# Optimization experiments

Hardware: AMD Instinct MI355X
Metric: run time of the kernel (lower is better)

The kernel has to match this reference:

```python
import jax, jax.numpy as jnp
import numpy as np

N = 100000   # nodes
E = 1600000  # edges
D_IN, H1, H2, H3 = 128, 128, 128, 64


def _sage_layer(x, src, dst, Wl, Wr, b):
    # PyG SAGEConv (aggr='mean'): out = lin_l(mean_{j in N(i)} x_j) + lin_r(x_i)
    msg_sum = jax.ops.segment_sum(x[src], dst, num_segments=N)          # [N, F]
    deg = jax.ops.segment_sum(jnp.ones((src.shape[0],), x.dtype), dst, num_segments=N)
    mean = msg_sum / jnp.clip(deg, 1.0)[:, None]
    return mean @ Wl + x @ Wr + b


def setup_inputs() -> dict:
    key = jax.random.key(0)
    ks = jax.random.split(key, 11)
    x = jax.random.normal(ks[0], (N, D_IN), dtype=jnp.float32)
    edge_index = jax.random.randint(ks[1], (2, E), 0, N, dtype=jnp.int32)

    def w(k, fin, fout):
        return jax.random.normal(k, (fin, fout), dtype=jnp.float32) * (1.0 / np.sqrt(fin))

    return {
        "x": x,
        "edge_index": edge_index,
        "W1_l": w(ks[2], D_IN, H1), "W1_r": w(ks[3], D_IN, H1), "b1": jnp.zeros((H1,), jnp.float32),
        "W2_l": w(ks[4], H1, H2),  "W2_r": w(ks[5], H1, H2),  "b2": jnp.zeros((H2,), jnp.float32),
        "W3_l": w(ks[6], H2, H3),  "W3_r": w(ks[7], H2, H3),  "b3": jnp.zeros((H3,), jnp.float32),
    }


def reference(x, edge_index, W1_l, W1_r, b1, W2_l, W2_r, b2, W3_l, W3_r, b3):
    src, dst = edge_index[0], edge_index[1]
    h = jax.nn.relu(_sage_layer(x, src, dst, W1_l, W1_r, b1))
    h = jax.nn.relu(_sage_layer(h, src, dst, W2_l, W2_r, b2))
    return _sage_layer(h, src, dst, W3_l, W3_r, b3)
```

## Files before the change

kernel.cpp:

```cpp
#include <hip/hip_runtime.h>

#define NN 100000
#define NE 1600000
#define NPB 256
#define NB 391
#define CAP 4864
#define NBLK_A 512
#define CHUNK_A (NE / NBLK_A)
#define CVT_N (NN * 16)

typedef __attribute__((ext_vector_type(8))) short bf16x8;
typedef __attribute__((ext_vector_type(4))) float f32x4;


__device__ __forceinline__ unsigned short f2bf(float f) {
    unsigned int u = __float_as_uint(f);
    unsigned int r = u + 0x7fffu + ((u >> 16) & 1u);
    return (unsigned short)(r >> 16);
}
__device__ __forceinline__ float bflo(unsigned int u) { return __uint_as_float(u << 16); }
__device__ __forceinline__ float bfhi(unsigned int u) { return __uint_as_float(u & 0xffff0000u); }
__device__ __forceinline__ unsigned int packbf(float lo, float hi) {
    return ((unsigned int)f2bf(hi) << 16) | (unsigned int)f2bf(lo);
}
__device__ __forceinline__ bf16x8 as_bf8(uint4 u) {
    union { uint4 u; bf16x8 h; } c;
    c.u = u;
    return c.h;
}


__global__ __launch_bounds__(256) void bucket_scatter_kernel(
    const int* __restrict__ src, const int* __restrict__ dst,
    int* __restrict__ gcur, unsigned* __restrict__ buckets) {
    __shared__ int hist[NB];
    __shared__ int base[NB];
    int t = threadIdx.x;
    for (int b = t; b < NB; b += 256) hist[b] = 0;
    __syncthreads();
    int e0 = blockIdx.x * CHUNK_A;
    for (int e = e0 + t; e < e0 + CHUNK_A; e += 256)
        atomicAdd(&hist[dst[e] >> 8], 1);
    __syncthreads();
    for (int b = t; b < NB; b += 256) {
        base[b] = atomicAdd(&gcur[b], hist[b]);
        hist[b] = 0;
    }
    __syncthreads();
    for (int e = e0 + t; e < e0 + CHUNK_A; e += 256) {
        int d = dst[e];
        int bkt = d >> 8;
        int slot = base[bkt] + atomicAdd(&hist[bkt], 1);
        if (slot < CAP)
            buckets[(size_t)bkt * CAP + slot] =
                ((unsigned)(d & 255) << 24) | (unsigned)src[e];
    }
}


__global__ __launch_bounds__(512) void bucket_scan_kernel(
    const int* __restrict__ gcur, int* __restrict__ bstart, int* __restrict__ row_ptr) {
    __shared__ int s[512];
    int t = threadIdx.x;
    int v = (t < NB) ? gcur[t] : 0;
    s[t] = v;
    __syncthreads();
    for (int off = 1; off < 512; off <<= 1) {
        int a = (t >= off) ? s[t - off] : 0;
        __syncthreads();
        s[t] += a;
        __syncthreads();
    }
    if (t < NB) bstart[t] = s[t] - v;
    if (t == NB - 1) {
        bstart[NB] = s[t];
        row_ptr[NN] = s[t];
    }
}


__global__ __launch_bounds__(256) void csr_finalize_kernel(
    const unsigned* __restrict__ buckets, const int* __restrict__ gcur,
    const int* __restrict__ bstart, int* __restrict__ row_ptr, int* __restrict__ adj) {
    __shared__ int hist[NPB];
    __shared__ int scn[NPB];
    int b = blockIdx.x;
    int t = threadIdx.x;
    int n = gcur[b];
    if (n > CAP) n = CAP;
    int base = bstart[b];
    const unsigned* bk = buckets + (size_t)b * CAP;

    hist[t] = 0;
    __syncthreads();
    for (int i = t; i < n; i += 256) atomicAdd(&hist[bk[i] >> 24], 1);
    __syncthreads();

    int v = hist[t];
    scn[t] = v;
    __syncthreads();
    for (int off = 1; off < 256; off <<= 1) {
        int add = (t >= off) ? scn[t - off] : 0;
        __syncthreads();
        scn[t] += add;
        __syncthreads();
    }
    int excl = scn[t] - v;
    int node = b * NPB + t;
    if (node < NN) row_ptr[node] = base + excl;

    hist[t] = excl;
    __syncthreads();
    for (int i = t; i < n; i += 256) {
        unsigned pr = bk[i];
        int pos = atomicAdd(&hist[pr >> 24], 1);
        adj[base + pos] = (int)(pr & 0xFFFFFFu);
    }
}


__device__ __forceinline__ void wfrag_one(const float* __restrict__ W, int H, int idx,
                                          uint4* __restrict__ out) {
    int lane = idx & 63;
    int tile = idx >> 6;
    int ntiles = H >> 4;
    int nt = tile % ntiles;
    int kt = tile / ntiles;
    int kbase = kt * 32 + (lane >> 4) * 8;
    int col = nt * 16 + (lane & 15);
    uint4 r;
    r.x = packbf(W[(size_t)(kbase + 0) * H + col], W[(size_t)(kbase + 1) * H + col]);
    r.y = packbf(W[(size_t)(kbase + 2) * H + col], W[(size_t)(kbase + 3) * H + col]);
    r.z = packbf(W[(size_t)(kbase + 4) * H + col], W[(size_t)(kbase + 5) * H + col]);
    r.w = packbf(W[(size_t)(kbase + 6) * H + col], W[(size_t)(kbase + 7) * H + col]);
    out[idx] = r;
}

__global__ __launch_bounds__(256) void prep_kernel(
    const float* __restrict__ x, unsigned int* __restrict__ x_bf,
    const float* __restrict__ W1l, const float* __restrict__ W1r,
    const float* __restrict__ W2l, const float* __restrict__ W2r,
    const float* __restrict__ W3l, const float* __restrict__ W3r,
    uint4* __restrict__ wf1, uint4* __restrict__ wf2,
    uint4* __restrict__ wf3l, uint4* __restrict__ wf3r) {
    int idx = blockIdx.x * blockDim.x + threadIdx.x;
    if (idx < CVT_N) {
        const float4* p = (const float4*)x + (size_t)idx * 2;
        float4 a = p[0], b = p[1];
        uint4 r;
        r.x = packbf(a.x, a.y);
        r.y = packbf(a.z, a.w);
        r.z = packbf(b.x, b.y);
        r.w = packbf(b.z, b.w);
        ((uint4*)x_bf)[idx] = r;
    } else {
        int k = idx - CVT_N;
        if (k < 2048)       wfrag_one(W1l, 128, k, wf1);
        else if (k < 4096)  wfrag_one(W1r, 128, k - 2048, wf1 + 2048);
        else if (k < 6144)  wfrag_one(W2l, 128, k - 4096, wf2);
        else if (k < 8192)  wfrag_one(W2r, 128, k - 6144, wf2 + 2048);
        else if (k < 9216)  wfrag_one(W3l, 64, k - 8192, wf3l);
        else if (k < 10240) wfrag_one(W3r, 64, k - 9216, wf3r);
    }
}


__global__ __launch_bounds__(128) void sage_fused_kernel(
    const uint4* __restrict__ xb4, const int* __restrict__ row_ptr,
    const int* __restrict__ adj, const uint4* __restrict__ wfrag,
    const float* __restrict__ bias, unsigned short* __restrict__ outb) {
    __shared__ uint4 As[32][17];

    const int w = threadIdx.x >> 6;
    const int l = threadIdx.x & 63;
    const int g = l >> 4;
    const int i = l & 15;
    const int r0 = blockIdx.x * 32 + w * 16;

    for (int wnode = 0; wnode < 16; ++wnode) {
        int node = r0 + wnode;
        float acc[8];
#pragma unroll
        for (int j = 0; j < 8; ++j) acc[j] = 0.f;
        int beg = row_ptr[node];
        int end = row_ptr[node + 1];
        int p = beg;
        for (; p + 16 <= end; p += 16) {
#pragma unroll
            for (int j = 0; j < 4; ++j) {
                int s = adj[p + j * 4 + g];
                uint4 u = xb4[(size_t)s * 16 + i];
                acc[0] += bflo(u.x);
                acc[1] += bfhi(u.x);
                acc[2] += bflo(u.y);
                acc[3] += bfhi(u.y);
                acc[4] += bflo(u.z);
                acc[5] += bfhi(u.z);
                acc[6] += bflo(u.w);
                acc[7] += bfhi(u.w);
            }
        }
        if (p < end) {
#pragma unroll
            for (int j = 0; j < 4; ++j) {
                int e = p + j * 4 + g;
                bool vv = e < end;
                int s = vv ? adj[e] : 0;
                uint4 u = xb4[(size_t)s * 16 + i];
                float m = vv ? 1.f : 0.f;
                acc[0] = fmaf(m, bflo(u.x), acc[0]);
                acc[1] = fmaf(m, bfhi(u.x), acc[1]);
                acc[2] = fmaf(m, bflo(u.y), acc[2]);
                acc[3] = fmaf(m, bfhi(u.y), acc[3]);
                acc[4] = fmaf(m, bflo(u.z), acc[4]);
                acc[5] = fmaf(m, bfhi(u.z), acc[5]);
                acc[6] = fmaf(m, bflo(u.w), acc[6]);
                acc[7] = fmaf(m, bfhi(u.w), acc[7]);
            }
        }
#pragma unroll
        for (int j = 0; j < 8; ++j) {
            acc[j] += __shfl_xor(acc[j], 16);
            acc[j] += __shfl_xor(acc[j], 32);
        }
        if (g == 0) {
            float inv = 1.0f / (float)(end > beg ? (end - beg) : 1);
            uint4 r;
            r.x = packbf(acc[0] * inv, acc[1] * inv);
            r.y = packbf(acc[2] * inv, acc[3] * inv);
            r.z = packbf(acc[4] * inv, acc[5] * inv);
            r.w = packbf(acc[6] * inv, acc[7] * inv);
            As[w * 16 + wnode][i] = r;
        }
    }

    const int arow = r0 + (l & 15);

    f32x4 acc[8];
#pragma unroll
    for (int nt = 0; nt < 8; ++nt) {
        f32x4 z = {0.f, 0.f, 0.f, 0.f};
        acc[nt] = z;
    }

#pragma unroll
    for (int kt = 0; kt < 4; ++kt) {
        bf16x8 av = as_bf8(As[w * 16 + (l & 15)][kt * 4 + g]);
#pragma unroll
        for (int nt = 0; nt < 8; ++nt) {
            bf16x8 bv = as_bf8(wfrag[(kt * 8 + nt) * 64 + l]);
            acc[nt] = __builtin_amdgcn_mfma_f32_16x16x32_bf16(av, bv, acc[nt], 0, 0, 0);
        }
    }
#pragma unroll
    for (int kt = 4; kt < 8; ++kt) {
        bf16x8 av = as_bf8(xb4[(size_t)arow * 16 + (kt & 3) * 4 + g]);
#pragma unroll
        for (int nt = 0; nt < 8; ++nt) {
            bf16x8 bv = as_bf8(wfrag[(kt * 8 + nt) * 64 + l]);
            acc[nt] = __builtin_amdgcn_mfma_f32_16x16x32_bf16(av, bv, acc[nt], 0, 0, 0);
        }
    }

    const int crow0 = r0 + ((l >> 4) << 2);
    const int ccol = l & 15;
#pragma unroll
    for (int nt = 0; nt < 8; ++nt) {
        float bb = bias[nt * 16 + ccol];
#pragma unroll
        for (int q = 0; q < 4; ++q) {
            int r = crow0 + q;
            float v = fmaxf(acc[nt][q] + bb, 0.f);
            outb[(size_t)r * 128 + nt * 16 + ccol] = f2bf(v);
        }
    }
}


__global__ __launch_bounds__(256) void mm64_mfma_kernel(
    const uint4* __restrict__ A, const uint4* __restrict__ wfrag,
    unsigned short* __restrict__ outb) {
    const int w = threadIdx.x >> 6;
    const int l = threadIdx.x & 63;
    const int r0 = blockIdx.x * 64 + w * 16;
    int arow = r0 + (l & 15);
    if (arow > NN - 1) arow = NN - 1;
    const int koff = l >> 4;

    f32x4 acc[4];
#pragma unroll
    for (int nt = 0; nt < 4; ++nt) {
        f32x4 z = {0.f, 0.f, 0.f, 0.f};
        acc[nt] = z;
    }

#pragma unroll
    for (int kt = 0; kt < 4; ++kt) {
        bf16x8 av = as_bf8(A[(size_t)arow * 16 + kt * 4 + koff]);
#pragma unroll
        for (int nt = 0; nt < 4; ++nt) {
            bf16x8 bv = as_bf8(wfrag[(kt * 4 + nt) * 64 + l]);
            acc[nt] = __builtin_amdgcn_mfma_f32_16x16x32_bf16(av, bv, acc[nt], 0, 0, 0);
        }
    }

    const int crow0 = r0 + ((l >> 4) << 2);
    const int ccol = l & 15;
#pragma unroll
    for (int nt = 0; nt < 4; ++nt) {
        int col = nt * 16 + ccol;
#pragma unroll
        for (int q = 0; q < 4; ++q) {
            int r = crow0 + q;
            if (r < NN) outb[(size_t)r * 64 + col] = f2bf(acc[nt][q]);
        }
    }
}


__global__ __launch_bounds__(128) void final_fused_kernel(
    const uint2* __restrict__ zb2, const int* __restrict__ row_ptr,
    const int* __restrict__ adj, const uint4* __restrict__ h2A,
    const uint4* __restrict__ wfrag, const float* __restrict__ bias,
    float* __restrict__ out) {
    __shared__ float As64[32][68];

    const int w = threadIdx.x >> 6;
    const int l = threadIdx.x & 63;
    const int g = l >> 4;
    const int i = l & 15;
    const int r0 = blockIdx.x * 32 + w * 16;

    for (int wnode = 0; wnode < 16; ++wnode) {
        int node = r0 + wnode;
        float acc[4];
#pragma unroll
        for (int j = 0; j < 4; ++j) acc[j] = 0.f;
        int beg = row_ptr[node];
        int end = row_ptr[node + 1];
        int p = beg;
        for (; p + 16 <= end; p += 16) {
#pragma unroll
            for (int j = 0; j < 4; ++j) {
                int s = adj[p + j * 4 + g];
                uint2 u = zb2[(size_t)s * 16 + i];
                acc[0] += bflo(u.x);
                acc[1] += bfhi(u.x);
                acc[2] += bflo(u.y);
                acc[3] += bfhi(u.y);
            }
        }
        if (p < end) {
#pragma unroll
            for (int j = 0; j < 4; ++j) {
                int e = p + j * 4 + g;
                bool vv = e < end;
                int s = vv ? adj[e] : 0;
                uint2 u = zb2[(size_t)s * 16 + i];
                float m = vv ? 1.f : 0.f;
                acc[0] = fmaf(m, bflo(u.x), acc[0]);
                acc[1] = fmaf(m, bfhi(u.x), acc[1]);
                acc[2] = fmaf(m, bflo(u.y), acc[2]);
                acc[3] = fmaf(m, bfhi(u.y), acc[3]);
            }
        }
#pragma unroll
        for (int j = 0; j < 4; ++j) {
            acc[j] += __shfl_xor(acc[j], 16);
            acc[j] += __shfl_xor(acc[j], 32);
        }
        if (g == 0) {
            float inv = 1.0f / (float)(end > beg ? (end - beg) : 1);
            float4 r;
            r.x = acc[0] * inv;
            r.y = acc[1] * inv;
            r.z = acc[2] * inv;
            r.w = acc[3] * inv;
            *(float4*)(&As64[w * 16 + wnode][i * 4]) = r;
        }
    }

    const int arow = r0 + (l & 15);

    f32x4 acc[4];
#pragma unroll
    for (int nt = 0; nt < 4; ++nt) {
        f32x4 z = {0.f, 0.f, 0.f, 0.f};
        acc[nt] = z;
    }

#pragma unroll
    for (int kt = 0; kt < 4; ++kt) {
        bf16x8 av = as_bf8(h2A[(size_t)arow * 16 + kt * 4 + g]);
#pragma unroll
        for (int nt = 0; nt < 4; ++nt) {
            bf16x8 bv = as_bf8(wfrag[(kt * 4 + nt) * 64 + l]);
            acc[nt] = __builtin_amdgcn_mfma_f32_16x16x32_bf16(av, bv, acc[nt], 0, 0, 0);
        }
    }

    const int lrow0 = (l >> 4) << 2;
    const int ccol = l & 15;
#pragma unroll
    for (int nt = 0; nt < 4; ++nt) {
        int col = nt * 16 + ccol;
        float bb = bias[col];
#pragma unroll
        for (int q = 0; q < 4; ++q) {
            int r = r0 + lrow0 + q;
            float v = acc[nt][q] + As64[w * 16 + lrow0 + q][col] + bb;
            out[(size_t)r * 64 + col] = v;
        }
    }
}


extern "C" void kernel_launch(void* const* d_in, const int* in_sizes, int n_in,
                              void* d_out, int out_size, void* d_ws, size_t ws_size,
                              hipStream_t stream) {
    (void)in_sizes; (void)n_in; (void)out_size; (void)ws_size;

    const float* x   = (const float*)d_in[0];
    const int* eidx  = (const int*)d_in[1];
    const int* src   = eidx;
    const int* dst   = eidx + NE;
    const float* W1l = (const float*)d_in[2];
    const float* W1r = (const float*)d_in[3];
    const float* b1  = (const float*)d_in[4];
    const float* W2l = (const float*)d_in[5];
    const float* W2r = (const float*)d_in[6];
    const float* b2  = (const float*)d_in[7];
    const float* W3l = (const float*)d_in[8];
    const float* W3r = (const float*)d_in[9];
    const float* b3  = (const float*)d_in[10];
    float* out = (float*)d_out;

    size_t off = 0;
    auto carve = [&](size_t bytes) -> void* {
        void* p = (char*)d_ws + off;
        off += (bytes + 255) & ~(size_t)255;
        return p;
    };
    int* gcur    = (int*)carve((size_t)NB * 4);
    int* bstart  = (int*)carve((size_t)(NB + 1) * 4);
    int* row_ptr = (int*)carve((size_t)(NN + 1) * 4);
    int* adj     = (int*)carve((size_t)NE * 4);
    unsigned* buckets = (unsigned*)carve((size_t)NB * CAP * 4);
    unsigned int* x_bf  = (unsigned int*)carve((size_t)NN * 64 * 4);
    unsigned int* h1_bf = (unsigned int*)carve((size_t)NN * 64 * 4);
    unsigned int* h2_bf = (unsigned int*)carve((size_t)NN * 64 * 4);
    unsigned int* z_bf  = (unsigned int*)carve((size_t)NN * 32 * 4);
    uint4* wf1  = (uint4*)carve((size_t)8 * 8 * 64 * 16);
    uint4* wf2  = (uint4*)carve((size_t)8 * 8 * 64 * 16);
    uint4* wf3l = (uint4*)carve((size_t)4 * 4 * 64 * 16);
    uint4* wf3r = (uint4*)carve((size_t)4 * 4 * 64 * 16);

    const int fgrid = NN / 32;
    const int mgrid = (NN + 63) / 64;
    const int pgrid = (CVT_N + 10240 + 255) / 256;

    hipMemsetAsync(gcur, 0, (size_t)NB * 4, stream);
    bucket_scatter_kernel<<<NBLK_A, 256, 0, stream>>>(src, dst, gcur, buckets);
    bucket_scan_kernel<<<1, 512, 0, stream>>>(gcur, bstart, row_ptr);
    csr_finalize_kernel<<<NB, 256, 0, stream>>>(buckets, gcur, bstart, row_ptr, adj);

    prep_kernel<<<pgrid, 256, 0, stream>>>(x, x_bf, W1l, W1r, W2l, W2r, W3l, W3r,
                                           wf1, wf2, wf3l, wf3r);

    sage_fused_kernel<<<fgrid, 128, 0, stream>>>((const uint4*)x_bf, row_ptr, adj,
                                                 wf1, b1, (unsigned short*)h1_bf);
    sage_fused_kernel<<<fgrid, 128, 0, stream>>>((const uint4*)h1_bf, row_ptr, adj,
                                                 wf2, b2, (unsigned short*)h2_bf);
    mm64_mfma_kernel<<<mgrid, 256, 0, stream>>>((const uint4*)h2_bf, wf3l,
                                                (unsigned short*)z_bf);
    final_fused_kernel<<<fgrid, 128, 0, stream>>>((const uint2*)z_bf, row_ptr, adj,
                                                  (const uint4*)h2_bf, wf3r, b3, out);
}
```

Baseline: 329.7 us.

## Split features into column slices and unfuse gather from MFMA projection

Node features are stored feature-major in 8 slices of 16 columns each. The neighbour gather runs as separate pull kernels, one block per 16 nodes and slice, so each slice (about 3.2MB) can stay cache-resident during the random gather. The MFMA projection moves into standalone kernels that read the aggregated buffer. This adds extra global round-trips for the aggregated features and more kernel launches, and each gather fetches only 8 bytes per lane, which lowers memory transaction efficiency.

After: 675.8 us. 105% more time.

```diff
diff --git a/kernel.cpp b/kernel.cpp
--- a/kernel.cpp
+++ b/kernel.cpp
@@ -7,7 +7,7 @@
 #define CAP 4864
 #define NBLK_A 512
 #define CHUNK_A (NE / NBLK_A)
-#define CVT_N (NN * 16)
+#define FM_N (NN * 16)
 
 typedef __attribute__((ext_vector_type(8))) short bf16x8;
 typedef __attribute__((ext_vector_type(4))) float f32x4;
@@ -137,24 +137,29 @@
 }
 
 __global__ __launch_bounds__(256) void prep_kernel(
-    const float* __restrict__ x, unsigned int* __restrict__ x_bf,
+    const float* __restrict__ x, uint4* __restrict__ xfm4,
     const float* __restrict__ W1l, const float* __restrict__ W1r,
     const float* __restrict__ W2l, const float* __restrict__ W2r,
     const float* __restrict__ W3l, const float* __restrict__ W3r,
     uint4* __restrict__ wf1, uint4* __restrict__ wf2,
     uint4* __restrict__ wf3l, uint4* __restrict__ wf3r) {
     int idx = blockIdx.x * blockDim.x + threadIdx.x;
-    if (idx < CVT_N) {
-        const float4* p = (const float4*)x + (size_t)idx * 2;
-        float4 a = p[0], b = p[1];
+    if (idx < FM_N) {
+        int c = idx / (NN * 2);
+        int rem = idx - c * (NN * 2);
+        int n = rem >> 1;
+        int h = rem & 1;
+        const float* p = x + (size_t)n * 128 + c * 16 + h * 8;
+        float4 a = *(const float4*)p;
+        float4 b = *(const float4*)(p + 4);
         uint4 r;
         r.x = packbf(a.x, a.y);
         r.y = packbf(a.z, a.w);
         r.z = packbf(b.x, b.y);
         r.w = packbf(b.z, b.w);
-        ((uint4*)x_bf)[idx] = r;
+        xfm4[((size_t)c * NN + n) * 2 + h] = r;
     } else {
-        int k = idx - CVT_N;
+        int k = idx - FM_N;
         if (k < 2048)       wfrag_one(W1l, 128, k, wf1);
         else if (k < 4096)  wfrag_one(W1r, 128, k - 2048, wf1 + 2048);
         else if (k < 6144)  wfrag_one(W2l, 128, k - 4096, wf2);
@@ -165,127 +170,158 @@
 }
 
 
-__global__ __launch_bounds__(128) void sage_fused_kernel(
-    const uint4* __restrict__ xb4, const int* __restrict__ row_ptr,
-    const int* __restrict__ adj, const uint4* __restrict__ wfrag,
-    const float* __restrict__ bias, unsigned short* __restrict__ outb) {
-    __shared__ uint4 As[32][17];
-
+__global__ __launch_bounds__(256) void pull128_fm_kernel(
+    const uint2* __restrict__ xfm2, const int* __restrict__ row_ptr,
+    const int* __restrict__ adj, uint2* __restrict__ agg2) {
+    const int c = blockIdx.x & 7;
+    const int ng = blockIdx.x >> 3;
     const int w = threadIdx.x >> 6;
     const int l = threadIdx.x & 63;
-    const int g = l >> 4;
-    const int i = l & 15;
-    const int r0 = blockIdx.x * 32 + w * 16;
-
-    for (int wnode = 0; wnode < 16; ++wnode) {
-        int node = r0 + wnode;
-        float acc[8];
-#pragma unroll
-        for (int j = 0; j < 8; ++j) acc[j] = 0.f;
-        int beg = row_ptr[node];
-        int end = row_ptr[node + 1];
-        int p = beg;
-        for (; p + 16 <= end; p += 16) {
-#pragma unroll
-            for (int j = 0; j < 4; ++j) {
-                int s = adj[p + j * 4 + g];
-                uint4 u = xb4[(size_t)s * 16 + i];
-                acc[0] += bflo(u.x);
-                acc[1] += bfhi(u.x);
-                acc[2] += bflo(u.y);
-                acc[3] += bfhi(u.y);
-                acc[4] += bflo(u.z);
-                acc[5] += bfhi(u.z);
-                acc[6] += bflo(u.w);
-                acc[7] += bfhi(u.w);
-            }
-        }
-        if (p < end) {
-#pragma unroll
-            for (int j = 0; j < 4; ++j) {
-                int e = p + j * 4 + g;
-                bool vv = e < end;
-                int s = vv ? adj[e] : 0;
-                uint4 u = xb4[(size_t)s * 16 + i];
-                float m = vv ? 1.f : 0.f;
-                acc[0] = fmaf(m, bflo(u.x), acc[0]);
-                acc[1] = fmaf(m, bfhi(u.x), acc[1]);
-                acc[2] = fmaf(m, bflo(u.y), acc[2]);
-                acc[3] = fmaf(m, bfhi(u.y), acc[3]);
-                acc[4] = fmaf(m, bflo(u.z), acc[4]);
-                acc[5] = fmaf(m, bfhi(u.z), acc[5]);
-                acc[6] = fmaf(m, bflo(u.w), acc[6]);
-                acc[7] = fmaf(m, bfhi(u.w), acc[7]);
-            }
-        }
-#pragma unroll
-        for (int j = 0; j < 8; ++j) {
-            acc[j] += __shfl_xor(acc[j], 16);
-            acc[j] += __shfl_xor(acc[j], 32);
-        }
-        if (g == 0) {
+    const int e = l & 15;
+    const int wd = l >> 4;
+    const uint2* slice = xfm2 + (size_t)c * NN * 4;
+
+#pragma unroll
+    for (int k = 0; k < 4; ++k) {
+        int node = ng * 16 + w * 4 + k;
+        int beg = row_ptr[node], end = row_ptr[node + 1];
+        float a0 = 0.f, a1 = 0.f, a2 = 0.f, a3 = 0.f;
+        for (int p = beg; p < end; p += 16) {
+            int ee = p + e;
+            bool v = ee < end;
+            int s = v ? adj[ee] : 0;
+            uint2 u = slice[(size_t)s * 4 + wd];
+            float m = v ? 1.f : 0.f;
+            a0 = fmaf(m, bflo(u.x), a0);
+            a1 = fmaf(m, bfhi(u.x), a1);
+            a2 = fmaf(m, bflo(u.y), a2);
+            a3 = fmaf(m, bfhi(u.y), a3);
+        }
+#pragma unroll
+        for (int msk = 1; msk < 16; msk <<= 1) {
+            a0 += __shfl_xor(a0, msk);
+            a1 += __shfl_xor(a1, msk);
+            a2 += __shfl_xor(a2, msk);
+            a3 += __shfl_xor(a3, msk);
+        }
+        if (e == 0) {
             float inv = 1.0f / (float)(end > beg ? (end - beg) : 1);
-            uint4 r;
-            r.x = packbf(acc[0] * inv, acc[1] * inv);
-            r.y = packbf(acc[2] * inv, acc[3] * inv);
-            r.z = packbf(acc[4] * inv, acc[5] * inv);
-            r.w = packbf(acc[6] * inv, acc[7] * inv);
-            As[w * 16 + wnode][i] = r;
-        }
-    }
-
-    const int arow = r0 + (l & 15);
-
-    f32x4 acc[8];
-#pragma unroll
-    for (int nt = 0; nt < 8; ++nt) {
-        f32x4 z = {0.f, 0.f, 0.f, 0.f};
-        acc[nt] = z;
-    }
-
-#pragma unroll
-    for (int kt = 0; kt < 4; ++kt) {
-        bf16x8 av = as_bf8(As[w * 16 + (l & 15)][kt * 4 + g]);
-#pragma unroll
-        for (int nt = 0; nt < 8; ++nt) {
-            bf16x8 bv = as_bf8(wfrag[(kt * 8 + nt) * 64 + l]);
-            acc[nt] = __builtin_amdgcn_mfma_f32_16x16x32_bf16(av, bv, acc[nt], 0, 0, 0);
-        }
-    }
-#pragma unroll
-    for (int kt = 4; kt < 8; ++kt) {
-        bf16x8 av = as_bf8(xb4[(size_t)arow * 16 + (kt & 3) * 4 + g]);
-#pragma unroll
-        for (int nt = 0; nt < 8; ++nt) {
-            bf16x8 bv = as_bf8(wfrag[(kt * 8 + nt) * 64 + l]);
-            acc[nt] = __builtin_amdgcn_mfma_f32_16x16x32_bf16(av, bv, acc[nt], 0, 0, 0);
-        }
-    }
-
-    const int crow0 = r0 + ((l >> 4) << 2);
-    const int ccol = l & 15;
-#pragma unroll
-    for (int nt = 0; nt < 8; ++nt) {
-        float bb = bias[nt * 16 + ccol];
-#pragma unroll
-        for (int q = 0; q < 4; ++q) {
-            int r = crow0 + q;
-            float v = fmaxf(acc[nt][q] + bb, 0.f);
-            outb[(size_t)r * 128 + nt * 16 + ccol] = f2bf(v);
-        }
-    }
-}
-
-
-__global__ __launch_bounds__(256) void mm64_mfma_kernel(
-    const uint4* __restrict__ A, const uint4* __restrict__ wfrag,
-    unsigned short* __restrict__ outb) {
+            uint2 r;
+            r.x = packbf(a0 * inv, a1 * inv);
+            r.y = packbf(a2 * inv, a3 * inv);
+            agg2[(size_t)node * 32 + c * 4 + wd] = r;
+        }
+    }
+}
+
+
+__global__ __launch_bounds__(256) void pull64_fm_kernel(
+    const unsigned* __restrict__ zfm1, const int* __restrict__ row_ptr,
+    const int* __restrict__ adj, float* __restrict__ agg3) {
+    const int c = blockIdx.x & 7;
+    const int ng = blockIdx.x >> 3;
+    const int w = threadIdx.x >> 6;
+    const int l = threadIdx.x & 63;
+    const int e = l & 15;
+    const int wd = l >> 4;
+    const unsigned* slice = zfm1 + (size_t)c * NN * 4;
+
+#pragma unroll
+    for (int k = 0; k < 4; ++k) {
+        int node = ng * 16 + w * 4 + k;
+        int beg = row_ptr[node], end = row_ptr[node + 1];
+        float a0 = 0.f, a1 = 0.f;
+        for (int p = beg; p < end; p += 16) {
+            int ee = p + e;
+            bool v = ee < end;
+            int s = v ? adj[ee] : 0;
+            unsigned u = slice[(size_t)s * 4 + wd];
+            float m = v ? 1.f : 0.f;
+            a0 = fmaf(m, bflo(u), a0);
+            a1 = fmaf(m, bfhi(u), a1);
+        }
+#pragma unroll
+        for (int msk = 1; msk < 16; msk <<= 1) {
+            a0 += __shfl_xor(a0, msk);
+            a1 += __shfl_xor(a1, msk);
+        }
+        if (e == 0) {
+            float inv = 1.0f / (float)(end > beg ? (end - beg) : 1);
+            float2 r;
+            r.x = a0 * inv;
+            r.y = a1 * inv;
+            *(float2*)(agg3 + (size_t)node * 64 + c * 8 + wd * 2) = r;
+        }
+    }
+}
+
+
+__global__ __launch_bounds__(256) void sage_mfma_kernel(
+    const uint4* __restrict__ agg4, const uint4* __restrict__ xfm4,
+    const uint4* __restrict__ wfrag, const float* __restrict__ bias,
+    unsigned short* __restrict__ outfm) {
     const int w = threadIdx.x >> 6;
     const int l = threadIdx.x & 63;
     const int r0 = blockIdx.x * 64 + w * 16;
     int arow = r0 + (l & 15);
     if (arow > NN - 1) arow = NN - 1;
-    const int koff = l >> 4;
+    const int g = l >> 4;
+
+    f32x4 acc[8];
+#pragma unroll
+    for (int nt = 0; nt < 8; ++nt) {
+        f32x4 z = {0.f, 0.f, 0.f, 0.f};
+        acc[nt] = z;
+    }
+
+#pragma unroll
+    for (int kt = 0; kt < 4; ++kt) {
+        bf16x8 av = as_bf8(agg4[(size_t)arow * 16 + kt * 4 + g]);
+#pragma unroll
+        for (int nt = 0; nt < 8; ++nt) {
+            bf16x8 bv = as_bf8(wfrag[(kt * 8 + nt) * 64 + l]);
+            acc[nt] = __builtin_amdgcn_mfma_f32_16x16x32_bf16(av, bv, acc[nt], 0, 0, 0);
+        }
+    }
+#pragma unroll
+    for (int kt = 4; kt < 8; ++kt) {
+        int c = 2 * (kt - 4) + (g >> 1);
+        bf16x8 av = as_bf8(xfm4[((size_t)c * NN + arow) * 2 + (g & 1)]);
+#pragma unroll
+        for (int nt = 0; nt < 8; ++nt) {
+            bf16x8 bv = as_bf8(wfrag[(kt * 8 + nt) * 64 + l]);
+            acc[nt] = __builtin_amdgcn_mfma_f32_16x16x32_bf16(av, bv, acc[nt], 0, 0, 0);
+        }
+    }
+
+    const int crow0 = r0 + ((l >> 4) << 2);
+    const int ccol = l & 15;
+#pragma unroll
+    for (int nt = 0; nt < 8; ++nt) {
+        float bb = bias[nt * 16 + ccol];
+#pragma unroll
+        for (int q = 0; q < 4; ++q) {
+            int r = crow0 + q;
+            if (r < NN) {
+                float v = fmaxf(acc[nt][q] + bb, 0.f);
+                outfm[((size_t)nt * NN + r) * 16 + ccol] = f2bf(v);
+            }
+        }
+    }
+}
+
+
+template <int MODE>
+__global__ __launch_bounds__(256) void mm64_mfma_kernel(
+    const uint4* __restrict__ hfm4, const uint4* __restrict__ wfrag,
+    const float* __restrict__ addin, const float* __restrict__ bias,
+    void* __restrict__ outp) {
+    const int w = threadIdx.x >> 6;
+    const int l = threadIdx.x & 63;
+    const int r0 = blockIdx.x * 64 + w * 16;
+    int arow = r0 + (l & 15);
+    if (arow > NN - 1) arow = NN - 1;
+    const int g = l >> 4;
 
     f32x4 acc[4];
 #pragma unroll
@@ -296,7 +332,8 @@
 
 #pragma unroll
     for (int kt = 0; kt < 4; ++kt) {
-        bf16x8 av = as_bf8(A[(size_t)arow * 16 + kt * 4 + koff]);
+        int c = 2 * kt + (g >> 1);
+        bf16x8 av = as_bf8(hfm4[((size_t)c * NN + arow) * 2 + (g & 1)]);
 #pragma unroll
         for (int nt = 0; nt < 4; ++nt) {
             bf16x8 bv = as_bf8(wfrag[(kt * 4 + nt) * 64 + l]);
@@ -312,104 +349,16 @@
 #pragma unroll
         for (int q = 0; q < 4; ++q) {
             int r = crow0 + q;
-            if (r < NN) outb[(size_t)r * 64 + col] = f2bf(acc[nt][q]);
-        }
-    }
-}
-
-
-__global__ __launch_bounds__(128) void final_fused_kernel(
-    const uint2* __restrict__ zb2, const int* __restrict__ row_ptr,
-    const int* __restrict__ adj, const uint4* __restrict__ h2A,
-    const uint4* __restrict__ wfrag, const float* __restrict__ bias,
-    float* __restrict__ out) {
-    __shared__ float As64[32][68];
-
-    const int w = threadIdx.x >> 6;
-    const int l = threadIdx.x & 63;
-    const int g = l >> 4;
-    const int i = l & 15;
-    const int r0 = blockIdx.x * 32 + w * 16;
-
-    for (int wnode = 0; wnode < 16; ++wnode) {
-        int node = r0 + wnode;
-        float acc[4];
-#pragma unroll
-        for (int j = 0; j < 4; ++j) acc[j] = 0.f;
-        int beg = row_ptr[node];
-        int end = row_ptr[node + 1];
-        int p = beg;
-        for (; p + 16 <= end; p += 16) {
-#pragma unroll
-            for (int j = 0; j < 4; ++j) {
-                int s = adj[p + j * 4 + g];
-                uint2 u = zb2[(size_t)s * 16 + i];
-                acc[0] += bflo(u.x);
-                acc[1] += bfhi(u.x);
-                acc[2] += bflo(u.y);
-                acc[3] += bfhi(u.y);
+            if (r < NN) {
+                if (MODE == 0) {
+                    int zc = 2 * nt + (ccol >> 3);
+                    ((unsigned short*)outp)[((size_t)zc * NN + r) * 8 + (ccol & 7)] =
+                        f2bf(acc[nt][q]);
+                } else {
+                    float v = acc[nt][q] + addin[(size_t)r * 64 + col] + bias[col];
+                    ((float*)outp)[(size_t)r * 64 + col] = v;
+                }
             }
-        }
-        if (p < end) {
-#pragma unroll
-            for (int j = 0; j < 4; ++j) {
-                int e = p + j * 4 + g;
-                bool vv = e < end;
-                int s = vv ? adj[e] : 0;
-                uint2 u = zb2[(size_t)s * 16 + i];
-                float m = vv ? 1.f : 0.f;
-                acc[0] = fmaf(m, bflo(u.x), acc[0]);
-                acc[1] = fmaf(m, bfhi(u.x), acc[1]);
-                acc[2] = fmaf(m, bflo(u.y), acc[2]);
-                acc[3] = fmaf(m, bfhi(u.y), acc[3]);
-            }
-        }
-#pragma unroll
-        for (int j = 0; j < 4; ++j) {
-            acc[j] += __shfl_xor(acc[j], 16);
-            acc[j] += __shfl_xor(acc[j], 32);
-        }
-        if (g == 0) {
-            float inv = 1.0f / (float)(end > beg ? (end - beg) : 1);
-            float4 r;
-            r.x = acc[0] * inv;
-            r.y = acc[1] * inv;
-            r.z = acc[2] * inv;
-            r.w = acc[3] * inv;
-            *(float4*)(&As64[w * 16 + wnode][i * 4]) = r;
-        }
-    }
-
-    const int arow = r0 + (l & 15);
-
-    f32x4 acc[4];
-#pragma unroll
-    for (int nt = 0; nt < 4; ++nt) {
-        f32x4 z = {0.f, 0.f, 0.f, 0.f};
-        acc[nt] = z;
-    }
-
-#pragma unroll
-    for (int kt = 0; kt < 4; ++kt) {
-        bf16x8 av = as_bf8(h2A[(size_t)arow * 16 + kt * 4 + g]);
-#pragma unroll
-        for (int nt = 0; nt < 4; ++nt) {
-            bf16x8 bv = as_bf8(wfrag[(kt * 4 + nt) * 64 + l]);
-            acc[nt] = __builtin_amdgcn_mfma_f32_16x16x32_bf16(av, bv, acc[nt], 0, 0, 0);
-        }
-    }
-
-    const int lrow0 = (l >> 4) << 2;
-    const int ccol = l & 15;
-#pragma unroll
-    for (int nt = 0; nt < 4; ++nt) {
-        int col = nt * 16 + ccol;
-        float bb = bias[col];
-#pragma unroll
-        for (int q = 0; q < 4; ++q) {
-            int r = r0 + lrow0 + q;
-            float v = acc[nt][q] + As64[w * 16 + lrow0 + q][col] + bb;
-            out[(size_t)r * 64 + col] = v;
         }
     }
 }
@@ -446,33 +395,39 @@
     int* row_ptr = (int*)carve((size_t)(NN + 1) * 4);
     int* adj     = (int*)carve((size_t)NE * 4);
     unsigned* buckets = (unsigned*)carve((size_t)NB * CAP * 4);
-    unsigned int* x_bf  = (unsigned int*)carve((size_t)NN * 64 * 4);
-    unsigned int* h1_bf = (unsigned int*)carve((size_t)NN * 64 * 4);
-    unsigned int* h2_bf = (unsigned int*)carve((size_t)NN * 64 * 4);
-    unsigned int* z_bf  = (unsigned int*)carve((size_t)NN * 32 * 4);
+    unsigned int* x_fm  = (unsigned int*)carve((size_t)NN * 64 * 4);
+    unsigned int* agg   = (unsigned int*)carve((size_t)NN * 64 * 4);
+    unsigned int* h1_fm = (unsigned int*)carve((size_t)NN * 64 * 4);
+    unsigned int* h2_fm = (unsigned int*)carve((size_t)NN * 64 * 4);
+    unsigned int* z_fm  = (unsigned int*)carve((size_t)NN * 32 * 4);
+    float* agg3         = (float*)carve((size_t)NN * 64 * 4);
     uint4* wf1  = (uint4*)carve((size_t)8 * 8 * 64 * 16);
     uint4* wf2  = (uint4*)carve((size_t)8 * 8 * 64 * 16);
     uint4* wf3l = (uint4*)carve((size_t)4 * 4 * 64 * 16);
     uint4* wf3r = (uint4*)carve((size_t)4 * 4 * 64 * 16);
 
-    const int fgrid = NN / 32;
+    const int pull_grid = (NN / 16) * 8;
     const int mgrid = (NN + 63) / 64;
-    const int pgrid = (CVT_N + 10240 + 255) / 256;
+    const int pgrid = (FM_N + 10240 + 255) / 256;
 
     hipMemsetAsync(gcur, 0, (size_t)NB * 4, stream);
     bucket_scatter_kernel<<<NBLK_A, 256, 0, stream>>>(src, dst, gcur, buckets);
     bucket_scan_kernel<<<1, 512, 0, stream>>>(gcur, bstart, row_ptr);
     csr_finalize_kernel<<<NB, 256, 0, stream>>>(buckets, gcur, bstart, row_ptr, adj);
 
-    prep_kernel<<<pgrid, 256, 0, stream>>>(x, x_bf, W1l, W1r, W2l, W2r, W3l, W3r,
+    prep_kernel<<<pgrid, 256, 0, stream>>>(x, (uint4*)x_fm, W1l, W1r, W2l, W2r, W3l, W3r,
                                            wf1, wf2, wf3l, wf3r);
 
-    sage_fused_kernel<<<fgrid, 128, 0, stream>>>((const uint4*)x_bf, row_ptr, adj,
-                                                 wf1, b1, (unsigned short*)h1_bf);
-    sage_fused_kernel<<<fgrid, 128, 0, stream>>>((const uint4*)h1_bf, row_ptr, adj,
-                                                 wf2, b2, (unsigned short*)h2_bf);
-    mm64_mfma_kernel<<<mgrid, 256, 0, stream>>>((const uint4*)h2_bf, wf3l,
-                                                (unsigned short*)z_bf);
-    final_fused_kernel<<<fgrid, 128, 0, stream>>>((const uint2*)z_bf, row_ptr, adj,
-                                                  (const uint4*)h2_bf, wf3r, b3, out);
-}
+    pull128_fm_kernel<<<pull_grid, 256, 0, stream>>>((const uint2*)x_fm, row_ptr, adj,
+                                                     (uint2*)agg);
+    sage_mfma_kernel<<<mgrid, 256, 0, stream>>>((const uint4*)agg, (const uint4*)x_fm,
+                                                wf1, b1, (unsigned short*)h1_fm);
+    pull128_fm_kernel<<<pull_grid, 256, 0, stream>>>((const uint2*)h1_fm, row_ptr, adj,
+                                                     (uint2*)agg);
+    sage_mfma_kernel<<<mgrid, 256, 0, stream>>>((const uint4*)agg, (const uint4*)h1_fm,
+                                                wf2, b2, (unsigned short*)h2_fm);
+    mm64_mfma_kernel<0><<<mgrid, 256, 0, stream>>>((const uint4*)h2_fm, wf3l,
+                                                   nullptr, nullptr, z_fm);
+    pull64_fm_kernel<<<pull_grid, 256, 0, stream>>>((const unsigned*)z_fm, row_ptr, adj, agg3);
+    mm64_mfma_kernel<1><<<mgrid, 256, 0, stream>>>((const uint4*)h2_fm, wf3r, agg3, b3, out);
+}
```

## Split fused gather+GEMM into separate pull and MFMA kernels, fuse layer-3 projection

Applied to the files above, without the earlier changes.

Replaces each fused per-block aggregate-then-MFMA kernel with a standalone pull kernel (one wave per node, many more blocks) that writes the mean aggregate to a workspace buffer, followed by a separate MFMA GEMM kernel. The layer-2 GEMM also computes the layer-3 left projection from LDS, which removes the standalone mm64 kernel. The final layer aggregates the projected features into an fp32 buffer and adds them in the right-projection kernel. The goal is better latency hiding in the irregular gather stage through higher parallelism. The cost is extra global round trips for the aggregate buffers and more kernel launches.

Result: faster. 300.6 us (-8.8%).

```diff
diff --git a/kernel.cpp b/kernel.cpp
--- a/kernel.cpp
+++ b/kernel.cpp
@@ -165,121 +165,134 @@
 }
 
 
-__global__ __launch_bounds__(128) void sage_fused_kernel(
+__global__ __launch_bounds__(256) void pull128_kernel(
     const uint4* __restrict__ xb4, const int* __restrict__ row_ptr,
-    const int* __restrict__ adj, const uint4* __restrict__ wfrag,
-    const float* __restrict__ bias, unsigned short* __restrict__ outb) {
-    __shared__ uint4 As[32][17];
-
-    const int w = threadIdx.x >> 6;
-    const int l = threadIdx.x & 63;
-    const int g = l >> 4;
-    const int i = l & 15;
-    const int r0 = blockIdx.x * 32 + w * 16;
-
-    for (int wnode = 0; wnode < 16; ++wnode) {
-        int node = r0 + wnode;
-        float acc[8];
-#pragma unroll
-        for (int j = 0; j < 8; ++j) acc[j] = 0.f;
-        int beg = row_ptr[node];
-        int end = row_ptr[node + 1];
-        int p = beg;
-        for (; p + 16 <= end; p += 16) {
-#pragma unroll
-            for (int j = 0; j < 4; ++j) {
-                int s = adj[p + j * 4 + g];
-                uint4 u = xb4[(size_t)s * 16 + i];
-                acc[0] += bflo(u.x);
-                acc[1] += bfhi(u.x);
-                acc[2] += bflo(u.y);
-                acc[3] += bfhi(u.y);
-                acc[4] += bflo(u.z);
-                acc[5] += bfhi(u.z);
-                acc[6] += bflo(u.w);
-                acc[7] += bfhi(u.w);
-            }
-        }
-        if (p < end) {
-#pragma unroll
-            for (int j = 0; j < 4; ++j) {
-                int e = p + j * 4 + g;
-                bool vv = e < end;
-                int s = vv ? adj[e] : 0;
-                uint4 u = xb4[(size_t)s * 16 + i];
-                float m = vv ? 1.f : 0.f;
-                acc[0] = fmaf(m, bflo(u.x), acc[0]);
-                acc[1] = fmaf(m, bfhi(u.x), acc[1]);
-                acc[2] = fmaf(m, bflo(u.y), acc[2]);
-                acc[3] = fmaf(m, bfhi(u.y), acc[3]);
-                acc[4] = fmaf(m, bflo(u.z), acc[4]);
-                acc[5] = fmaf(m, bfhi(u.z), acc[5]);
-                acc[6] = fmaf(m, bflo(u.w), acc[6]);
-                acc[7] = fmaf(m, bfhi(u.w), acc[7]);
-            }
-        }
-#pragma unroll
-        for (int j = 0; j < 8; ++j) {
-            acc[j] += __shfl_xor(acc[j], 16);
-            acc[j] += __shfl_xor(acc[j], 32);
-        }
-        if (g == 0) {
-            float inv = 1.0f / (float)(end > beg ? (end - beg) : 1);
-            uint4 r;
-            r.x = packbf(acc[0] * inv, acc[1] * inv);
-            r.y = packbf(acc[2] * inv, acc[3] * inv);
-            r.z = packbf(acc[4] * inv, acc[5] * inv);
-            r.w = packbf(acc[6] * inv, acc[7] * inv);
-            As[w * 16 + wnode][i] = r;
-        }
-    }
-
-    const int arow = r0 + (l & 15);
-
-    f32x4 acc[8];
-#pragma unroll
-    for (int nt = 0; nt < 8; ++nt) {
-        f32x4 z = {0.f, 0.f, 0.f, 0.f};
-        acc[nt] = z;
-    }
-
-#pragma unroll
-    for (int kt = 0; kt < 4; ++kt) {
-        bf16x8 av = as_bf8(As[w * 16 + (l & 15)][kt * 4 + g]);
-#pragma unroll
-        for (int nt = 0; nt < 8; ++nt) {
-            bf16x8 bv = as_bf8(wfrag[(kt * 8 + nt) * 64 + l]);
-            acc[nt] = __builtin_amdgcn_mfma_f32_16x16x32_bf16(av, bv, acc[nt], 0, 0, 0);
-        }
-    }
-#pragma unroll
-    for (int kt = 4; kt < 8; ++kt) {
-        bf16x8 av = as_bf8(xb4[(size_t)arow * 16 + (kt & 3) * 4 + g]);
-#pragma unroll
-        for (int nt = 0; nt < 8; ++nt) {
-            bf16x8 bv = as_bf8(wfrag[(kt * 8 + nt) * 64 + l]);
-            acc[nt] = __builtin_amdgcn_mfma_f32_16x16x32_bf16(av, bv, acc[nt], 0, 0, 0);
-        }
-    }
-
-    const int crow0 = r0 + ((l >> 4) << 2);
-    const int ccol = l & 15;
-#pragma unroll
-    for (int nt = 0; nt < 8; ++nt) {
-        float bb = bias[nt * 16 + ccol];
-#pragma unroll
-        for (int q = 0; q < 4; ++q) {
-            int r = crow0 + q;
-            float v = fmaxf(acc[nt][q] + bb, 0.f);
-            outb[(size_t)r * 128 + nt * 16 + ccol] = f2bf(v);
-        }
-    }
-}
-
-
-__global__ __launch_bounds__(256) void mm64_mfma_kernel(
-    const uint4* __restrict__ A, const uint4* __restrict__ wfrag,
-    unsigned short* __restrict__ outb) {
+    const int* __restrict__ adj, uint4* __restrict__ aggb4) {
+    int node = blockIdx.x * 4 + (threadIdx.x >> 6);
+    int l = threadIdx.x & 63;
+    int g = l >> 4;
+    int i = l & 15;
+    int beg = row_ptr[node], end = row_ptr[node + 1];
+    float acc[8];
+#pragma unroll
+    for (int j = 0; j < 8; ++j) acc[j] = 0.f;
+
+    int p = beg;
+    for (; p + 16 <= end; p += 16) {
+#pragma unroll
+        for (int j = 0; j < 4; ++j) {
+            int s = adj[p + j * 4 + g];
+            uint4 u = xb4[(size_t)s * 16 + i];
+            acc[0] += bflo(u.x);
+            acc[1] += bfhi(u.x);
+            acc[2] += bflo(u.y);
+            acc[3] += bfhi(u.y);
+            acc[4] += bflo(u.z);
+            acc[5] += bfhi(u.z);
+            acc[6] += bflo(u.w);
+            acc[7] += bfhi(u.w);
+        }
+    }
+    if (p < end) {
+#pragma unroll
+        for (int j = 0; j < 4; ++j) {
+            int e = p + j * 4 + g;
+            bool vv = e < end;
+            int s = vv ? adj[e] : 0;
+            uint4 u = xb4[(size_t)s * 16 + i];
+            float m = vv ? 1.f : 0.f;
+            acc[0] = fmaf(m, bflo(u.x), acc[0]);
+            acc[1] = fmaf(m, bfhi(u.x), acc[1]);
+            acc[2] = fmaf(m, bflo(u.y), acc[2]);
+            acc[3] = fmaf(m, bfhi(u.y), acc[3]);
+            acc[4] = fmaf(m, bflo(u.z), acc[4]);
+            acc[5] = fmaf(m, bfhi(u.z), acc[5]);
+            acc[6] = fmaf(m, bflo(u.w), acc[6]);
+            acc[7] = fmaf(m, bfhi(u.w), acc[7]);
+        }
+    }
+
+#pragma unroll
+    for (int j = 0; j < 8; ++j) {
+        acc[j] += __shfl_xor(acc[j], 16);
+        acc[j] += __shfl_xor(acc[j], 32);
+    }
+    if (g == 0) {
+        float inv = 1.0f / (float)(end > beg ? (end - beg) : 1);
+        uint4 r;
+        r.x = packbf(acc[0] * inv, acc[1] * inv);
+        r.y = packbf(acc[2] * inv, acc[3] * inv);
+        r.z = packbf(acc[4] * inv, acc[5] * inv);
+        r.w = packbf(acc[6] * inv, acc[7] * inv);
+        aggb4[(size_t)node * 16 + i] = r;
+    }
+}
+
+
+__global__ __launch_bounds__(256) void pull64_kernel(
+    const uint2* __restrict__ zb2, const int* __restrict__ row_ptr,
+    const int* __restrict__ adj, float* __restrict__ aggout) {
+    int node = blockIdx.x * 4 + (threadIdx.x >> 6);
+    int l = threadIdx.x & 63;
+    int g = l >> 4;
+    int i = l & 15;
+    int beg = row_ptr[node], end = row_ptr[node + 1];
+    float acc[4];
+#pragma unroll
+    for (int j = 0; j < 4; ++j) acc[j] = 0.f;
+
+    int p = beg;
+    for (; p + 16 <= end; p += 16) {
+#pragma unroll
+        for (int j = 0; j < 4; ++j) {
+            int s = adj[p + j * 4 + g];
+            uint2 u = zb2[(size_t)s * 16 + i];
+            acc[0] += bflo(u.x);
+            acc[1] += bfhi(u.x);
+            acc[2] += bflo(u.y);
+            acc[3] += bfhi(u.y);
+        }
+    }
+    if (p < end) {
+#pragma unroll
+        for (int j = 0; j < 4; ++j) {
+            int e = p + j * 4 + g;
+            bool vv = e < end;
+            int s = vv ? adj[e] : 0;
+            uint2 u = zb2[(size_t)s * 16 + i];
+            float m = vv ? 1.f : 0.f;
+            acc[0] = fmaf(m, bflo(u.x), acc[0]);
+            acc[1] = fmaf(m, bfhi(u.x), acc[1]);
+            acc[2] = fmaf(m, bflo(u.y), acc[2]);
+            acc[3] = fmaf(m, bfhi(u.y), acc[3]);
+        }
+    }
+
+#pragma unroll
+    for (int j = 0; j < 4; ++j) {
+        acc[j] += __shfl_xor(acc[j], 16);
+        acc[j] += __shfl_xor(acc[j], 32);
+    }
+    if (g == 0) {
+        float inv = 1.0f / (float)(end > beg ? (end - beg) : 1);
+        float4 r;
+        r.x = acc[0] * inv;
+        r.y = acc[1] * inv;
+        r.z = acc[2] * inv;
+        r.w = acc[3] * inv;
+        *(float4*)(aggout + (size_t)node * 64 + i * 4) = r;
+    }
+}
+
+
+template <bool FUSE_Z>
+__global__ __launch_bounds__(256) void sage_mfma_kernel(
+    const uint4* __restrict__ aggA, const uint4* __restrict__ xinA,
+    const uint4* __restrict__ wfrag, const float* __restrict__ bias,
+    unsigned short* __restrict__ outb,
+    const uint4* __restrict__ wfz, unsigned short* __restrict__ zout) {
+    extern __shared__ unsigned short hts[];
+
     const int w = threadIdx.x >> 6;
     const int l = threadIdx.x & 63;
     const int r0 = blockIdx.x * 64 + w * 16;
@@ -287,6 +300,83 @@
     if (arow > NN - 1) arow = NN - 1;
     const int koff = l >> 4;
 
+    f32x4 acc[8];
+#pragma unroll
+    for (int nt = 0; nt < 8; ++nt) {
+        f32x4 z = {0.f, 0.f, 0.f, 0.f};
+        acc[nt] = z;
+    }
+
+#pragma unroll
+    for (int kt = 0; kt < 8; ++kt) {
+        const uint4* Ab = (kt < 4) ? aggA : xinA;
+        const int ktl = kt & 3;
+        bf16x8 av = as_bf8(Ab[(size_t)arow * 16 + ktl * 4 + koff]);
+#pragma unroll
+        for (int nt = 0; nt < 8; ++nt) {
+            bf16x8 bv = as_bf8(wfrag[(kt * 8 + nt) * 64 + l]);
+            acc[nt] = __builtin_amdgcn_mfma_f32_16x16x32_bf16(av, bv, acc[nt], 0, 0, 0);
+        }
+    }
+
+    const int crow0 = r0 + ((l >> 4) << 2);
+    const int ccol = l & 15;
+#pragma unroll
+    for (int nt = 0; nt < 8; ++nt) {
+        float bb = bias[nt * 16 + ccol];
+#pragma unroll
+        for (int q = 0; q < 4; ++q) {
+            int r = crow0 + q;
+            unsigned short hb = f2bf(fmaxf(acc[nt][q] + bb, 0.f));
+            if (r < NN) outb[(size_t)r * 128 + nt * 16 + ccol] = hb;
+            if (FUSE_Z) {
+                hts[((size_t)w * 16 + ((l >> 4) << 2) + q) * 136 + nt * 16 + ccol] = hb;
+            }
+        }
+    }
+
+    if (FUSE_Z) {
+        __syncthreads();
+        f32x4 accz[4];
+#pragma unroll
+        for (int nt = 0; nt < 4; ++nt) {
+            f32x4 z = {0.f, 0.f, 0.f, 0.f};
+            accz[nt] = z;
+        }
+#pragma unroll
+        for (int kt = 0; kt < 4; ++kt) {
+            const uint4 hv =
+                *(const uint4*)&hts[((size_t)w * 16 + (l & 15)) * 136 + kt * 32 + (l >> 4) * 8];
+            bf16x8 av = as_bf8(hv);
+#pragma unroll
+            for (int nt = 0; nt < 4; ++nt) {
+                bf16x8 bv = as_bf8(wfz[(kt * 4 + nt) * 64 + l]);
+                accz[nt] = __builtin_amdgcn_mfma_f32_16x16x32_bf16(av, bv, accz[nt], 0, 0, 0);
+            }
+        }
+#pragma unroll
+        for (int nt = 0; nt < 4; ++nt) {
+#pragma unroll
+            for (int q = 0; q < 4; ++q) {
+                int r = crow0 + q;
+                if (r < NN) zout[(size_t)r * 64 + nt * 16 + ccol] = f2bf(accz[nt][q]);
+            }
+        }
+    }
+}
+
+
+__global__ __launch_bounds__(256) void mm64_final_kernel(
+    const uint4* __restrict__ A, const uint4* __restrict__ wfrag,
+    const float* __restrict__ addin, const float* __restrict__ bias,
+    float* __restrict__ out) {
+    const int w = threadIdx.x >> 6;
+    const int l = threadIdx.x & 63;
+    const int r0 = blockIdx.x * 64 + w * 16;
+    int arow = r0 + (l & 15);
+    if (arow > NN - 1) arow = NN - 1;
+    const int koff = l >> 4;
+
     f32x4 acc[4];
 #pragma unroll
     for (int nt = 0; nt < 4; ++nt) {
@@ -312,104 +402,10 @@
 #pragma unroll
         for (int q = 0; q < 4; ++q) {
             int r = crow0 + q;
-            if (r < NN) outb[(size_t)r * 64 + col] = f2bf(acc[nt][q]);
-        }
-    }
-}
-
-
-__global__ __launch_bounds__(128) void final_fused_kernel(
-    const uint2* __restrict__ zb2, const int* __restrict__ row_ptr,
-    const int* __restrict__ adj, const uint4* __restrict__ h2A,
-    const uint4* __restrict__ wfrag, const float* __restrict__ bias,
-    float* __restrict__ out) {
-    __shared__ float As64[32][68];
-
-    const int w = threadIdx.x >> 6;
-    const int l = threadIdx.x & 63;
-    const int g = l >> 4;
-    const int i = l & 15;
-    const int r0 = blockIdx.x * 32 + w * 16;
-
-    for (int wnode = 0; wnode < 16; ++wnode) {
-        int node = r0 + wnode;
-        float acc[4];
-#pragma unroll
-        for (int j = 0; j < 4; ++j) acc[j] = 0.f;
-        int beg = row_ptr[node];
-        int end = row_ptr[node + 1];
-        int p = beg;
-        for (; p + 16 <= end; p += 16) {
-#pragma unroll
-            for (int j = 0; j < 4; ++j) {
-                int s = adj[p + j * 4 + g];
-                uint2 u = zb2[(size_t)s * 16 + i];
-                acc[0] += bflo(u.x);
-                acc[1] += bfhi(u.x);
-                acc[2] += bflo(u.y);
-                acc[3] += bfhi(u.y);
+            if (r < NN) {
+                out[(size_t)r * 64 + col] =
+                    acc[nt][q] + addin[(size_t)r * 64 + col] + bias[col];
             }
-        }
-        if (p < end) {
-#pragma unroll
-            for (int j = 0; j < 4; ++j) {
-                int e = p + j * 4 + g;
-                bool vv = e < end;
-                int s = vv ? adj[e] : 0;
-                uint2 u = zb2[(size_t)s * 16 + i];
-                float m = vv ? 1.f : 0.f;
-                acc[0] = fmaf(m, bflo(u.x), acc[0]);
-                acc[1] = fmaf(m, bfhi(u.x), acc[1]);
-                acc[2] = fmaf(m, bflo(u.y), acc[2]);
-                acc[3] = fmaf(m, bfhi(u.y), acc[3]);
-            }
-        }
-#pragma unroll
-        for (int j = 0; j < 4; ++j) {
-            acc[j] += __shfl_xor(acc[j], 16);
-            acc[j] += __shfl_xor(acc[j], 32);
-        }
-        if (g == 0) {
-            float inv = 1.0f / (float)(end > beg ? (end - beg) : 1);
-            float4 r;
-            r.x = acc[0] * inv;
-            r.y = acc[1] * inv;
-            r.z = acc[2] * inv;
-            r.w = acc[3] * inv;
-            *(float4*)(&As64[w * 16 + wnode][i * 4]) = r;
-        }
-    }
-
-    const int arow = r0 + (l & 15);
-
-    f32x4 acc[4];
-#pragma unroll
-    for (int nt = 0; nt < 4; ++nt) {
-        f32x4 z = {0.f, 0.f, 0.f, 0.f};
-        acc[nt] = z;
-    }
-
-#pragma unroll
-    for (int kt = 0; kt < 4; ++kt) {
-        bf16x8 av = as_bf8(h2A[(size_t)arow * 16 + kt * 4 + g]);
-#pragma unroll
-        for (int nt = 0; nt < 4; ++nt) {
-            bf16x8 bv = as_bf8(wfrag[(kt * 4 + nt) * 64 + l]);
-            acc[nt] = __builtin_amdgcn_mfma_f32_16x16x32_bf16(av, bv, acc[nt], 0, 0, 0);
-        }
-    }
-
-    const int lrow0 = (l >> 4) << 2;
-    const int ccol = l & 15;
-#pragma unroll
-    for (int nt = 0; nt < 4; ++nt) {
-        int col = nt * 16 + ccol;
-        float bb = bias[col];
-#pragma unroll
-        for (int q = 0; q < 4; ++q) {
-            int r = r0 + lrow0 + q;
-            float v = acc[nt][q] + As64[w * 16 + lrow0 + q][col] + bb;
-            out[(size_t)r * 64 + col] = v;
         }
     }
 }
@@ -447,32 +443,36 @@
     int* adj     = (int*)carve((size_t)NE * 4);
     unsigned* buckets = (unsigned*)carve((size_t)NB * CAP * 4);
     unsigned int* x_bf  = (unsigned int*)carve((size_t)NN * 64 * 4);
+    unsigned int* agg   = (unsigned int*)carve((size_t)NN * 64 * 4);
     unsigned int* h1_bf = (unsigned int*)carve((size_t)NN * 64 * 4);
     unsigned int* h2_bf = (unsigned int*)carve((size_t)NN * 64 * 4);
     unsigned int* z_bf  = (unsigned int*)carve((size_t)NN * 32 * 4);
+    float* agg3         = (float*)carve((size_t)NN * 64 * 4);
     uint4* wf1  = (uint4*)carve((size_t)8 * 8 * 64 * 16);
     uint4* wf2  = (uint4*)carve((size_t)8 * 8 * 64 * 16);
     uint4* wf3l = (uint4*)carve((size_t)4 * 4 * 64 * 16);
     uint4* wf3r = (uint4*)carve((size_t)4 * 4 * 64 * 16);
 
-    const int fgrid = NN / 32;
+    const int pgrid = (NN + 3) / 4;
     const int mgrid = (NN + 63) / 64;
-    const int pgrid = (CVT_N + 10240 + 255) / 256;
+    const int cgrid = (CVT_N + 10240) / 256;
 
     hipMemsetAsync(gcur, 0, (size_t)NB * 4, stream);
     bucket_scatter_kernel<<<NBLK_A, 256, 0, stream>>>(src, dst, gcur, buckets);
     bucket_scan_kernel<<<1, 512, 0, stream>>>(gcur, bstart, row_ptr);
     csr_finalize_kernel<<<NB, 256, 0, stream>>>(buckets, gcur, bstart, row_ptr, adj);
 
-    prep_kernel<<<pgrid, 256, 0, stream>>>(x, x_bf, W1l, W1r, W2l, W2r, W3l, W3r,
+    prep_kernel<<<cgrid, 256, 0, stream>>>(x, x_bf, W1l, W1r, W2l, W2r, W3l, W3r,
                                            wf1, wf2, wf3l, wf3r);
 
-    sage_fused_kernel<<<fgrid, 128, 0, stream>>>((const uint4*)x_bf, row_ptr, adj,
-                                                 wf1, b1, (unsigned short*)h1_bf);
-    sage_fused_kernel<<<fgrid, 128, 0, stream>>>((const uint4*)h1_bf, row_ptr, adj,
-                                                 wf2, b2, (unsigned short*)h2_bf);
-    mm64_mfma_kernel<<<mgrid, 256, 0, stream>>>((const uint4*)h2_bf, wf3l,
-                                                (unsigned short*)z_bf);
-    final_fused_kernel<<<fgrid, 128, 0, stream>>>((const uint2*)z_bf, row_ptr, adj,
-                                                  (const uint4*)h2_bf, wf3r, b3, out);
-}
+    pull128_kernel<<<pgrid, 256, 0, stream>>>((const uint4*)x_bf, row_ptr, adj, (uint4*)agg);
+    sage_mfma_kernel<false><<<mgrid, 256, 0, stream>>>(
+        (const uint4*)agg, (const uint4*)x_bf, wf1, b1, (unsigned short*)h1_bf,
+        nullptr, nullptr);
+    pull128_kernel<<<pgrid, 256, 0, stream>>>((const uint4*)h1_bf, row_ptr, adj, (uint4*)agg);
+    sage_mfma_kernel<true><<<mgrid, 256, 4 * 16 * 136 * 2, stream>>>(
+        (const uint4*)agg, (const uint4*)h1_bf, wf2, b2, (unsigned short*)h2_bf,
+        wf3l, (unsigned short*)z_bf);
+    pull64_kernel<<<pgrid, 256, 0, stream>>>((const uint2*)z_bf, row_ptr, adj, agg3);
+    mm64_final_kernel<<<mgrid, 256, 0, stream>>>((const uint4*)h2_bf, wf3r, agg3, b3, out);
+}
```
